# Performance work log

Hardware: AMD Instinct MI355X
Metric: run time of the kernel (lower is better)

Reference implementation:

```python
import jax, jax.numpy as jnp
import numpy as np

IN_DIM = 768   # 256 + 256 + 128 + 128
OUT_DIM = 256
N_EDGES = 320000
N_GRAPHS = 64


def setup_inputs() -> dict:
    key = jax.random.key(0)
    ks = jax.random.split(key, 7)
    src = jax.random.normal(ks[0], (N_EDGES, 256), dtype=jnp.float32)
    dest = jax.random.normal(ks[1], (N_EDGES, 256), dtype=jnp.float32)
    edge_attr = jax.random.normal(ks[2], (N_EDGES, 128), dtype=jnp.float32)
    u = jax.random.normal(ks[3], (N_GRAPHS, 128), dtype=jnp.float32)
    batch = jnp.sort(jax.random.randint(ks[4], (N_EDGES,), 0, N_GRAPHS, dtype=jnp.int64)) if jax.config.read('jax_enable_x64') else jnp.sort(jax.random.randint(ks[4], (N_EDGES,), 0, N_GRAPHS)).astype(jnp.int32)
    # Linear(in_dim, out_dim): torch default init ~ U(-1/sqrt(in), 1/sqrt(in))
    bound = 1.0 / np.sqrt(IN_DIM)
    W = jax.random.uniform(ks[5], (IN_DIM, OUT_DIM), dtype=jnp.float32, minval=-bound, maxval=bound)
    b = jax.random.uniform(ks[6], (OUT_DIM,), dtype=jnp.float32, minval=-bound, maxval=bound)
    return {"src": src, "dest": dest, "edge_attr": edge_attr, "u": u, "batch": batch, "W": W, "b": b}


def reference(src, dest, edge_attr, u, batch, W, b):
    # u_expanded = u[batch]; concat [dest, src, edge_attr, u_exp]; Linear + ReLU
    u_exp = jnp.take(u, batch, axis=0)                    # [E, 128]
    combined = jnp.concatenate([dest, src, edge_attr, u_exp], axis=1)  # [E, 768]
    out = combined @ W + b                                # [E, 256]
    return jax.nn.relu(out)
```

## Files before the change

### kernel.cpp

```cpp
#include <hip/hip_runtime.h>
#include <cstdint>
#include <cstddef>

#define BM 128
#define BN 256
#define BK 32
#define KT_STEPS 24
#define THREADS 512
#define LDS_A_BYTES (BM * BK * 2)

typedef __attribute__((ext_vector_type(4))) float f32x4;
typedef __attribute__((ext_vector_type(8))) short bf16x8;

__device__ __forceinline__ unsigned short f2bf(float f) {
  union { float f; uint32_t u; } v; v.f = f;
  uint32_t r = v.u + 0x7FFFu + ((v.u >> 16) & 1u);
  return (unsigned short)(r >> 16);
}

__device__ __forceinline__ bf16x8 cvt8(f32x4 a, f32x4 b) {
  bf16x8 r;
  r[0] = (short)f2bf(a[0]); r[1] = (short)f2bf(a[1]);
  r[2] = (short)f2bf(a[2]); r[3] = (short)f2bf(a[3]);
  r[4] = (short)f2bf(b[0]); r[5] = (short)f2bf(b[1]);
  r[6] = (short)f2bf(b[2]); r[7] = (short)f2bf(b[3]);
  return r;
}

__global__ void wt_kernel(const float* __restrict__ W, unsigned short* __restrict__ WtS) {
  const int gid = blockIdx.x * 256 + threadIdx.x;
  const int kt = gid >> 10;
  const int c  = gid & 1023;
  const int n  = ((c >> 6) << 4) | (c & 15);
  const int k0 = kt * 32 + ((c >> 4) & 3) * 8;
  float v[8];
#pragma unroll
  for (int i = 0; i < 8; ++i) v[i] = W[(size_t)(k0 + i) * 256 + n];
  f32x4 a = {v[0], v[1], v[2], v[3]};
  f32x4 b = {v[4], v[5], v[6], v[7]};
  *(bf16x8*)((char*)WtS + (size_t)gid * 16) = cvt8(a, b);
}

__global__ __launch_bounds__(THREADS, 4) void edge_gemm(
    const float* __restrict__ srcf, const float* __restrict__ destf,
    const float* __restrict__ eaf, const float* __restrict__ uf,
    const int* __restrict__ batch, const unsigned short* __restrict__ WtS,
    const float* __restrict__ bias, float* __restrict__ out)
{
  __shared__ char smem[2 * LDS_A_BYTES];
  const int tid  = threadIdx.x;
  const int lane = tid & 63;
  const int w    = tid >> 6;
  const int wr   = w >> 2;
  const int wc   = w & 3;
  const int m0   = blockIdx.x * BM;
  const int l15  = lane & 15;
  const int l4   = lane >> 4;

  const int ar = w * 16 + (tid & 15);
  const int aq = (tid >> 4) & 3;
  const int ae = m0 + ar;

  float bs[4];
#pragma unroll
  for (int nf = 0; nf < 4; ++nf) bs[nf] = bias[wc * 64 + nf * 16 + l15];

  f32x4 acc[4][4];
  f32x4 z = {0.f, 0.f, 0.f, 0.f};
#pragma unroll
  for (int i = 0; i < 4; ++i)
#pragma unroll
    for (int j = 0; j < 4; ++j) acc[i][j] = z;

  auto a_ptr = [&](int kt) -> const float* {
    const int coff = aq * 8;
    if (kt < 8)  return destf + (size_t)ae * 256 + kt * 32 + coff;
    if (kt < 16) return srcf  + (size_t)ae * 256 + (kt - 8) * 32 + coff;
    if (kt < 20) return eaf   + (size_t)ae * 128 + (kt - 16) * 32 + coff;
    return uf + (size_t)batch[ae] * 128 + (kt - 20) * 32 + coff;
  };

  f32x4 va0, va1;
  auto load_a = [&](int kt) {
    const float* p = a_ptr(kt);
    va0 = *(const f32x4*)(p);
    va1 = *(const f32x4*)(p + 4);
  };
  auto write_a = [&](int buf) {
    char* Ab = smem + buf * LDS_A_BYTES;
    *(bf16x8*)(Ab + w * 1024 + lane * 16) = cvt8(va0, va1);
  };

  bf16x8 bfr[4];
  auto load_b = [&](int kt) {
    const char* wb = (const char*)WtS + (size_t)kt * 16384;
#pragma unroll
    for (int nf = 0; nf < 4; ++nf)
      bfr[nf] = *(const bf16x8*)(wb + ((wc * 4 + nf) * 64 + l4 * 16 + l15) * 16);
  };

  auto compute = [&](int buf) {
    const char* Ab = smem + buf * LDS_A_BYTES;
    bf16x8 af[4];
#pragma unroll
    for (int mf = 0; mf < 4; ++mf)
      af[mf] = *(const bf16x8*)(Ab + (wr * 4 + mf) * 1024 + l4 * 256 + l15 * 16);
#pragma unroll
    for (int mf = 0; mf < 4; ++mf)
#pragma unroll
      for (int nf = 0; nf < 4; ++nf)
        acc[mf][nf] = __builtin_amdgcn_mfma_f32_16x16x32_bf16(
            af[mf], bfr[nf], acc[mf][nf], 0, 0, 0);
  };

  load_a(0);
  write_a(0);
  __syncthreads();

  int cur = 0;
  for (int kt = 0; kt < KT_STEPS; ++kt) {
    const bool more = (kt + 1 < KT_STEPS);
    load_b(kt);
    if (more) load_a(kt + 1);
    compute(cur);
    if (more) write_a(cur ^ 1);
    __syncthreads();
    cur ^= 1;
  }

#pragma unroll
  for (int mf = 0; mf < 4; ++mf) {
    const int r0 = m0 + wr * 64 + mf * 16 + l4 * 4;
#pragma unroll
    for (int nf = 0; nf < 4; ++nf) {
      const int cn = wc * 64 + nf * 16 + l15;
      const f32x4 v = acc[mf][nf];
#pragma unroll
      for (int j = 0; j < 4; ++j) {
        const float x = v[j] + bs[nf];
        out[(size_t)(r0 + j) * 256 + cn] = x > 0.f ? x : 0.f;
      }
    }
  }
}

extern "C" void kernel_launch(void* const* d_in, const int* in_sizes, int n_in,
                              void* d_out, int out_size, void* d_ws, size_t ws_size,
                              hipStream_t stream) {
  const float* srcf  = (const float*)d_in[0];
  const float* destf = (const float*)d_in[1];
  const float* eaf   = (const float*)d_in[2];
  const float* uf    = (const float*)d_in[3];
  const int*   batch = (const int*)d_in[4];
  const float* W     = (const float*)d_in[5];
  const float* bias  = (const float*)d_in[6];
  float* out = (float*)d_out;
  unsigned short* WtS = (unsigned short*)d_ws;

  wt_kernel<<<96, 256, 0, stream>>>(W, WtS);

  edge_gemm<<<320000 / BM, THREADS, 0, stream>>>(
      srcf, destf, eaf, uf, batch, WtS, bias, out);
}
```

Measured before the change: 292.8 us.

## Triple-buffer A and B tiles in LDS with async global_load_lds for weights

Halves the M tile to 64 rows and moves the bf16 weight tile into LDS using direct global-to-LDS loads. A and B now share a three-stage LDS ring, prefetched two steps ahead and guarded by explicit waitcnt plus barrier. The batch index is loaded once per thread, and the fp32-to-bf16 packing now produces 32-bit words. This aims to hide global latency and shrink per-wave register pressure, at the cost of more blocks, a smaller tile with less reuse, and fragile hand-counted vmcnt synchronisation.

After: 282.0 us. 1.04x faster.

```diff
diff --git a/kernel.cpp b/kernel.cpp
--- a/kernel.cpp
+++ b/kernel.cpp
@@ -2,29 +2,24 @@
 #include <cstdint>
 #include <cstddef>
 
-#define BM 128
+#define BM 64
 #define BN 256
 #define BK 32
-#define KT_STEPS 24
+#define NT 24
 #define THREADS 512
-#define LDS_A_BYTES (BM * BK * 2)
+#define A_BYTES (BM * BK * 2)
+#define B_BYTES (BN * BK * 2)
+#define BUF_BYTES (A_BYTES + B_BYTES)
+#define NBUF 3
 
 typedef __attribute__((ext_vector_type(4))) float f32x4;
 typedef __attribute__((ext_vector_type(8))) short bf16x8;
+typedef __attribute__((ext_vector_type(2))) unsigned int u32x2;
 
-__device__ __forceinline__ unsigned short f2bf(float f) {
+__device__ __forceinline__ unsigned int f2bf(float f) {
   union { float f; uint32_t u; } v; v.f = f;
   uint32_t r = v.u + 0x7FFFu + ((v.u >> 16) & 1u);
-  return (unsigned short)(r >> 16);
-}
-
-__device__ __forceinline__ bf16x8 cvt8(f32x4 a, f32x4 b) {
-  bf16x8 r;
-  r[0] = (short)f2bf(a[0]); r[1] = (short)f2bf(a[1]);
-  r[2] = (short)f2bf(a[2]); r[3] = (short)f2bf(a[3]);
-  r[4] = (short)f2bf(b[0]); r[5] = (short)f2bf(b[1]);
-  r[6] = (short)f2bf(b[2]); r[7] = (short)f2bf(b[3]);
-  return r;
+  return r >> 16;
 }
 
 __global__ void wt_kernel(const float* __restrict__ W, unsigned short* __restrict__ WtS) {
@@ -33,12 +28,13 @@
   const int c  = gid & 1023;
   const int n  = ((c >> 6) << 4) | (c & 15);
   const int k0 = kt * 32 + ((c >> 4) & 3) * 8;
-  float v[8];
+  unsigned int p[4];
 #pragma unroll
-  for (int i = 0; i < 8; ++i) v[i] = W[(size_t)(k0 + i) * 256 + n];
-  f32x4 a = {v[0], v[1], v[2], v[3]};
-  f32x4 b = {v[4], v[5], v[6], v[7]};
-  *(bf16x8*)((char*)WtS + (size_t)gid * 16) = cvt8(a, b);
+  for (int i = 0; i < 4; ++i)
+    p[i] = f2bf(W[(size_t)(k0 + 2 * i) * 256 + n]) |
+           (f2bf(W[(size_t)(k0 + 2 * i + 1) * 256 + n]) << 16);
+  *(u32x2*)((char*)WtS + (size_t)gid * 16)     = u32x2{p[0], p[1]};
+  *(u32x2*)((char*)WtS + (size_t)gid * 16 + 8) = u32x2{p[2], p[3]};
 }
 
 __global__ __launch_bounds__(THREADS, 4) void edge_gemm(
@@ -47,7 +43,7 @@
     const int* __restrict__ batch, const unsigned short* __restrict__ WtS,
     const float* __restrict__ bias, float* __restrict__ out)
 {
-  __shared__ char smem[2 * LDS_A_BYTES];
+  __shared__ char smem[NBUF * BUF_BYTES];
   const int tid  = threadIdx.x;
   const int lane = tid & 63;
   const int w    = tid >> 6;
@@ -57,80 +53,98 @@
   const int l15  = lane & 15;
   const int l4   = lane >> 4;
 
-  const int ar = w * 16 + (tid & 15);
-  const int aq = (tid >> 4) & 3;
-  const int ae = m0 + ar;
+  const int s_row  = ((tid >> 7) << 4) | ((tid >> 1) & 15);
+  const int s_coff = (((tid >> 5) & 3) << 3) | ((tid & 1) << 2);
+  const int s_ae   = m0 + s_row;
+  const int s_ub   = batch[s_ae];
 
   float bs[4];
 #pragma unroll
   for (int nf = 0; nf < 4; ++nf) bs[nf] = bias[wc * 64 + nf * 16 + l15];
 
-  f32x4 acc[4][4];
+  f32x4 acc[2][4];
   f32x4 z = {0.f, 0.f, 0.f, 0.f};
 #pragma unroll
-  for (int i = 0; i < 4; ++i)
+  for (int i = 0; i < 2; ++i)
 #pragma unroll
     for (int j = 0; j < 4; ++j) acc[i][j] = z;
 
   auto a_ptr = [&](int kt) -> const float* {
-    const int coff = aq * 8;
-    if (kt < 8)  return destf + (size_t)ae * 256 + kt * 32 + coff;
-    if (kt < 16) return srcf  + (size_t)ae * 256 + (kt - 8) * 32 + coff;
-    if (kt < 20) return eaf   + (size_t)ae * 128 + (kt - 16) * 32 + coff;
-    return uf + (size_t)batch[ae] * 128 + (kt - 20) * 32 + coff;
+    if (kt < 8)  return destf + (size_t)s_ae * 256 + kt * 32 + s_coff;
+    if (kt < 16) return srcf  + (size_t)s_ae * 256 + (kt - 8) * 32 + s_coff;
+    if (kt < 20) return eaf   + (size_t)s_ae * 128 + (kt - 16) * 32 + s_coff;
+    return uf + (size_t)s_ub * 128 + (kt - 20) * 32 + s_coff;
   };
 
-  f32x4 va0, va1;
-  auto load_a = [&](int kt) {
-    const float* p = a_ptr(kt);
-    va0 = *(const f32x4*)(p);
-    va1 = *(const f32x4*)(p + 4);
+  f32x4 va[2];
+
+  auto stage = [&](int kt) {
+    char* Bb = smem + (kt % NBUF) * BUF_BYTES + A_BYTES;
+    const char* wb = (const char*)WtS + (size_t)kt * B_BYTES;
+#pragma unroll
+    for (int j = 0; j < 2; ++j) {
+      const char* g = wb + (size_t)(j * 512 + tid) * 16;
+      char* l = Bb + (size_t)(j * 512 + w * 64) * 16;
+      __builtin_amdgcn_global_load_lds(
+          (const __attribute__((address_space(1))) uint32_t*)g,
+          (__attribute__((address_space(3))) uint32_t*)l, 16, 0, 0);
+    }
+    va[kt & 1] = *(const f32x4*)a_ptr(kt);
   };
-  auto write_a = [&](int buf) {
-    char* Ab = smem + buf * LDS_A_BYTES;
-    *(bf16x8*)(Ab + w * 1024 + lane * 16) = cvt8(va0, va1);
+  auto write_a = [&](int kt) {
+    char* Ab = smem + (kt % NBUF) * BUF_BYTES;
+    f32x4 v = va[kt & 1];
+    u32x2 p;
+    p[0] = f2bf(v[0]) | (f2bf(v[1]) << 16);
+    p[1] = f2bf(v[2]) | (f2bf(v[3]) << 16);
+    *(u32x2*)(Ab + tid * 8) = p;
   };
-
-  bf16x8 bfr[4];
-  auto load_b = [&](int kt) {
-    const char* wb = (const char*)WtS + (size_t)kt * 16384;
+  auto compute = [&](int kt) {
+    const char* Ab = smem + (kt % NBUF) * BUF_BYTES;
+    const char* Bb = Ab + A_BYTES;
+    bf16x8 af[2], bfr[4];
+#pragma unroll
+    for (int mf = 0; mf < 2; ++mf)
+      af[mf] = *(const bf16x8*)(Ab + (((wr * 2 + mf) * 64) + l4 * 16 + l15) * 16);
 #pragma unroll
     for (int nf = 0; nf < 4; ++nf)
-      bfr[nf] = *(const bf16x8*)(wb + ((wc * 4 + nf) * 64 + l4 * 16 + l15) * 16);
-  };
-
-  auto compute = [&](int buf) {
-    const char* Ab = smem + buf * LDS_A_BYTES;
-    bf16x8 af[4];
+      bfr[nf] = *(const bf16x8*)(Bb + (((wc * 4 + nf) * 64) + l4 * 16 + l15) * 16);
 #pragma unroll
-    for (int mf = 0; mf < 4; ++mf)
-      af[mf] = *(const bf16x8*)(Ab + (wr * 4 + mf) * 1024 + l4 * 256 + l15 * 16);
-#pragma unroll
-    for (int mf = 0; mf < 4; ++mf)
+    for (int mf = 0; mf < 2; ++mf)
 #pragma unroll
       for (int nf = 0; nf < 4; ++nf)
         acc[mf][nf] = __builtin_amdgcn_mfma_f32_16x16x32_bf16(
             af[mf], bfr[nf], acc[mf][nf], 0, 0, 0);
   };
 
-  load_a(0);
+#define STEP_SYNC()                                          \
+  asm volatile("s_waitcnt vmcnt(3)" ::: "memory");           \
+  __builtin_amdgcn_sched_barrier(0);                         \
+  asm volatile("s_waitcnt lgkmcnt(0)" ::: "memory");         \
+  __builtin_amdgcn_sched_barrier(0);                         \
+  __builtin_amdgcn_s_barrier()
+
+  stage(0);
+  __builtin_amdgcn_sched_barrier(0);
+  stage(1);
+  __builtin_amdgcn_sched_barrier(0);
   write_a(0);
-  __syncthreads();
+  STEP_SYNC();
 
-  int cur = 0;
-  for (int kt = 0; kt < KT_STEPS; ++kt) {
-    const bool more = (kt + 1 < KT_STEPS);
-    load_b(kt);
-    if (more) load_a(kt + 1);
-    compute(cur);
-    if (more) write_a(cur ^ 1);
-    __syncthreads();
-    cur ^= 1;
+#pragma unroll
+  for (int kt = 0; kt < NT; ++kt) {
+    if (kt + 2 < NT) stage(kt + 2);
+    __builtin_amdgcn_sched_barrier(0);
+    compute(kt);
+    if (kt + 1 < NT) {
+      write_a(kt + 1);
+      STEP_SYNC();
+    }
   }
 
 #pragma unroll
-  for (int mf = 0; mf < 4; ++mf) {
-    const int r0 = m0 + wr * 64 + mf * 16 + l4 * 4;
+  for (int mf = 0; mf < 2; ++mf) {
+    const int r0 = m0 + wr * 32 + mf * 16 + l4 * 4;
 #pragma unroll
     for (int nf = 0; nf < 4; ++nf) {
       const int cn = wc * 64 + nf * 16 + l15;
@@ -142,6 +156,7 @@
       }
     }
   }
+#undef STEP_SYNC
 }
 
 extern "C" void kernel_launch(void* const* d_in, const int* in_sizes, int n_in,
```
